# Kernel tuning notes

Measured on AMD Instinct MI355X. Metric: run time of the kernel, lower is better.

Reference implementation:

```python
import jax, jax.numpy as jnp
import numpy as np

B, N, IN_DIM, D, H = 8, 2048, 256, 512, 4
HD = D // H
GX, GY = 8, 8
IMG_W, IMG_H = 256.0, 256.0
CW, CH = IMG_W / GX, IMG_H / GY
NBH = 1
EPS = 1e-5


def setup_inputs() -> dict:
    key = jax.random.key(0)
    ks = jax.random.split(key, 12)
    s = 0.02
    rn = lambda k, sh: jax.random.normal(k, sh, jnp.float32) * s
    return {
        'features': jax.random.normal(ks[0], (B, N, IN_DIM), jnp.float32),
        'coords': jax.random.uniform(ks[1], (B, N, 2), jnp.float32) * IMG_W,
        'W_feat': rn(ks[2], (IN_DIM, D)), 'b_feat': jnp.zeros((D,), jnp.float32),
        'W_p1': rn(ks[3], (2, D // 2)), 'b_p1': jnp.zeros((D // 2,), jnp.float32),
        'W_p2': rn(ks[4], (D // 2, D)), 'b_p2': jnp.zeros((D,), jnp.float32),
        'Wq': rn(ks[5], (D, D)), 'bq': jnp.zeros((D,), jnp.float32),
        'Wk': rn(ks[6], (D, D)), 'bk': jnp.zeros((D,), jnp.float32),
        'Wv': rn(ks[7], (D, D)), 'bv': jnp.zeros((D,), jnp.float32),
        'Wo': rn(ks[8], (D, D)), 'bo': jnp.zeros((D,), jnp.float32),
        'gamma': jnp.ones((D,), jnp.float32), 'beta': jnp.zeros((D,), jnp.float32),
    }


def reference(features, coords, W_feat, b_feat, W_p1, b_p1, W_p2, b_p2,
              Wq, bq, Wk, bk, Wv, bv, Wo, bo, gamma, beta):
    feat = features @ W_feat + b_feat                          # [B,N,D]
    # --- grid bucketing (mean feature per occupied cell) ---
    gx = jnp.clip((coords[..., 0] / CW).astype(jnp.int32), 0, GX - 1)
    gy = jnp.clip((coords[..., 1] / CH).astype(jnp.int32), 0, GY - 1)
    cell = gx * GY + gy                                        # [B,N]
    G = GX * GY
    seg = (jnp.arange(B, dtype=jnp.int32)[:, None] * G + cell).reshape(-1)
    sums = jax.ops.segment_sum(feat.reshape(B * N, D), seg, num_segments=B * G)
    counts = jax.ops.segment_sum(jnp.ones((B * N,), jnp.float32), seg, num_segments=B * G)
    mean = (sums / jnp.maximum(counts, 1.0)[:, None]).reshape(B, G, D)
    counts = counts.reshape(B, G)
    # --- neighbor cells (static 3x3 window for neighborhood=1) ---
    offs = np.array([(dx, dy) for dx in range(-NBH, NBH + 1) for dy in range(-NBH, NBH + 1)], np.int32)
    K = offs.shape[0]
    pe = jnp.asarray(offs, jnp.float32)
    pe = jax.nn.relu(pe @ W_p1 + b_p1) @ W_p2 + b_p2           # [K,D] pos enc of offsets
    ngx = gx[..., None] + offs[:, 0]                           # [B,N,K]
    ngy = gy[..., None] + offs[:, 1]
    inb = (ngx >= 0) & (ngx < GX) & (ngy >= 0) & (ngy < GY)
    nidx = jnp.clip(ngx, 0, GX - 1) * GY + jnp.clip(ngy, 0, GY - 1)
    bidx = jnp.arange(B)[:, None, None]
    valid = inb & (counts[bidx, nidx] > 0)                     # [B,N,K]
    keys = mean[bidx, nidx] + pe                               # [B,N,K,D]
    # --- per-point attention over <=9 neighbor cells ---
    q = (feat @ Wq + bq).reshape(B, N, H, HD)
    k = (keys @ Wk + bk).reshape(B, N, K, H, HD)
    v = (keys @ Wv + bv).reshape(B, N, K, H, HD)
    scores = jnp.einsum('bnhd,bnkhd->bnhk', q, k) / np.float32(np.sqrt(HD))
    scores = jnp.where(valid[:, :, None, :], scores, jnp.float32(-1e9))
    attn = jax.nn.softmax(scores, axis=-1)
    agg = jnp.einsum('bnhk,bnkhd->bnhd', attn, v).reshape(B, N, D) @ Wo + bo
    enhanced = feat + agg                                      # residual (dropout in eval = identity)
    mu = enhanced.mean(-1, keepdims=True)
    var = enhanced.var(-1, keepdims=True)
    return (enhanced - mu) / jnp.sqrt(var + EPS) * gamma + beta
```

## Files before the change

kernel.cpp:

```cpp
#include <hip/hip_runtime.h>
#include <stdint.h>

typedef unsigned short u16;
typedef unsigned int u32;
typedef __bf16 bf16x8 __attribute__((ext_vector_type(8)));
typedef float f32x4 __attribute__((ext_vector_type(4)));

#define NBATCH 8
#define NPT    2048
#define NPTS   16384
#define INDIM  256
#define DD     512
#define GG     64

__device__ __forceinline__ u16 f2bf(float f){
  u32 u = __builtin_bit_cast(u32, f);
  u += 0x7fffu + ((u >> 16) & 1u);
  return (u16)(u >> 16);
}
__device__ __forceinline__ float bf2f(u16 h){
  u32 u = ((u32)h) << 16;
  return __builtin_bit_cast(float, u);
}
__device__ __forceinline__ void load8(const float* __restrict__ p, float* r){
  float4 a = *(const float4*)p;
  float4 b = *(const float4*)(p + 4);
  r[0]=a.x;r[1]=a.y;r[2]=a.z;r[3]=a.w;r[4]=b.x;r[5]=b.y;r[6]=b.z;r[7]=b.w;
}
__device__ __forceinline__ void load8bf(const u16* __restrict__ p, float* r){
  uint4 v = *(const uint4*)p;
  r[0]=bf2f((u16)v.x); r[1]=bf2f((u16)(v.x>>16));
  r[2]=bf2f((u16)v.y); r[3]=bf2f((u16)(v.y>>16));
  r[4]=bf2f((u16)v.z); r[5]=bf2f((u16)(v.z>>16));
  r[6]=bf2f((u16)v.w); r[7]=bf2f((u16)(v.w>>16));
}
__device__ __forceinline__ void store8(float* __restrict__ p, const float* r){
  float4 a; a.x=r[0];a.y=r[1];a.z=r[2];a.w=r[3];
  float4 b; b.x=r[4];b.y=r[5];b.z=r[6];b.w=r[7];
  *(float4*)p = a; *(float4*)(p+4) = b;
}
__device__ __forceinline__ uint4 pack8(const float* a){
  uint4 pk;
  pk.x = (u32)f2bf(a[0]) | ((u32)f2bf(a[1]) << 16);
  pk.y = (u32)f2bf(a[2]) | ((u32)f2bf(a[3]) << 16);
  pk.z = (u32)f2bf(a[4]) | ((u32)f2bf(a[5]) << 16);
  pk.w = (u32)f2bf(a[6]) | ((u32)f2bf(a[7]) << 16);
  return pk;
}
typedef __attribute__((address_space(1))) unsigned as1u;
typedef __attribute__((address_space(3))) unsigned as3u;
__device__ __forceinline__ void gload16(const void* g, void* l){
  __builtin_amdgcn_global_load_lds((as1u*)(uintptr_t)g, (as3u*)(uintptr_t)l, 16, 0, 0);
}

__device__ __forceinline__ void transpose64(const float* __restrict__ src, int scols,
                                            u16* __restrict__ dst, int dcols,
                                            int r0, int c0, char* smem, int t){
  float (*sh)[65] = (float(*)[65])smem;
  #pragma unroll
  for (int i = 0; i < 16; i++){
    int idx = i*256 + t;
    int r = idx >> 6, c = idx & 63;
    sh[r][c] = src[(size_t)(r0 + r)*scols + c0 + c];
  }
  __syncthreads();
  #pragma unroll
  for (int i = 0; i < 8; i++){
    int idx = i*512 + t*2;
    int oR = idx >> 6, oC = idx & 63;
    u32 pk = (u32)f2bf(sh[oC][oR]) | ((u32)f2bf(sh[oC+1][oR]) << 16);
    *(u32*)(dst + (size_t)(c0 + oR)*dcols + r0 + oC) = pk;
  }
}

#define P_R1 2048
#define P_R2 2112
#define P_R3 2368
#define P_R4 2400
#define P_R5 2409
#define P_R6 2411
#define P_R7 2415
#define P_NB 2423
__global__ __launch_bounds__(256) void prep_kernel(
    const float* __restrict__ features, const float* __restrict__ W_feat,
    const float* __restrict__ Wq, const float* __restrict__ Wk,
    const float* __restrict__ Wv, const float* __restrict__ Wo,
    const float* __restrict__ W_p1, const float* __restrict__ b_p1,
    const float* __restrict__ W_p2, const float* __restrict__ b_p2,
    const float* __restrict__ b_feat, const float* __restrict__ bq,
    const float* __restrict__ bk, const float* __restrict__ bv,
    const float* __restrict__ coords,
    u16* __restrict__ featA, u16* __restrict__ W_feat_bf,
    u16* __restrict__ WqkvT, u16* __restrict__ WoT, u16* __restrict__ WcatT,
    u16* __restrict__ peD, float* __restrict__ bfq, float* __restrict__ biaskv,
    int* __restrict__ order, int* __restrict__ counts, int* __restrict__ cellstart)
{
  __shared__ __align__(16) char smem[34048];
  int bid = blockIdx.x, t = threadIdx.x;
  if (bid < P_R1){
    int i = bid*256 + t;
    float r[8]; load8(features + (size_t)i*8, r);
    *(uint4*)(featA + (size_t)i*8) = pack8(r);
  } else if (bid < P_R2){
    int i = (bid - P_R1)*256 + t;
    float r[8]; load8(W_feat + (size_t)i*8, r);
    *(uint4*)(W_feat_bf + (size_t)i*8) = pack8(r);
  } else if (bid < P_R3){
    int rel = bid - P_R2;
    int mat = rel >> 6, tile = rel & 63;
    int r0 = (tile >> 3)*64, c0 = (tile & 7)*64;
    const float* src = mat==0 ? Wq : (mat==1 ? Wk : (mat==2 ? Wv : Wo));
    u16* dst = mat==0 ? WqkvT : (mat==1 ? WqkvT + (size_t)512*DD
                     : (mat==2 ? WqkvT + (size_t)1024*DD : WoT));
    transpose64(src, DD, dst, DD, r0, c0, smem, t);
  } else if (bid < P_R4){
    int rel = bid - P_R3;
    int r0 = (rel >> 3)*64, c0 = (rel & 7)*64;
    transpose64(W_feat, DD, WcatT, INDIM, r0, c0, smem, t);
  } else if (bid < P_R5){
    int kk = bid - P_R4;
    float dx = (float)(kk/3 - 1), dy = (float)(kk%3 - 1);
    float* h = (float*)smem;
    float hv = dx*W_p1[t] + dy*W_p1[256 + t] + b_p1[t];
    h[t] = hv > 0.f ? hv : 0.f;
    __syncthreads();
    float acc0 = b_p2[t], acc1 = b_p2[t + 256];
    for (int c = 0; c < 256; c++){
      float hc = h[c];
      acc0 += hc * W_p2[(size_t)c*DD + t];
      acc1 += hc * W_p2[(size_t)c*DD + t + 256];
    }
    peD[(size_t)kk*DD + t]       = f2bf(acc0);
    peD[(size_t)kk*DD + t + 256] = f2bf(acc1);
  } else if (bid < P_R6){
    int i = (bid - P_R5)*256 + t;
    float* bfs = (float*)smem;
    bfs[t] = b_feat[t]; bfs[t + 256] = b_feat[t + 256];
    __syncthreads();
    float acc = 0.f;
    for (int k = 0; k < DD; k++) acc += bfs[k] * Wq[(size_t)k*DD + i];
    bfq[i] = acc + bq[i];
  } else if (bid < P_R7){
    int n = (bid - P_R6)*256 + t;
    float* bfs = (float*)smem;
    bfs[t] = b_feat[t]; bfs[t + 256] = b_feat[t + 256];
    __syncthreads();
    const float* W = (n < 512) ? Wk : Wv;
    int c = n & 511;
    float acc = 0.f;
    for (int k = 0; k < DD; k++) acc += bfs[k] * W[(size_t)k*DD + c];
    biaskv[n] = acc + ((n < 512) ? bk[c] : bv[c]);
  } else {
    int b = bid - P_R7;
    u16 (*hist)[65] = (u16(*)[65])smem;
    int* tot  = (int*)(smem + 33280);
    int* base = (int*)(smem + 33536);
    #pragma unroll
    for (int i = 0; i < 65; i++) hist[t][i] = 0;
    int myc[8];
    float cxy[16];
    load8(coords + (size_t)(b*NPT + t*8)*2,     cxy);
    load8(coords + (size_t)(b*NPT + t*8)*2 + 8, cxy + 8);
    #pragma unroll
    for (int i = 0; i < 8; i++){
      int gx = (int)(cxy[2*i]   * (1.0f/32.0f)); gx = gx < 0 ? 0 : (gx > 7 ? 7 : gx);
      int gy = (int)(cxy[2*i+1] * (1.0f/32.0f)); gy = gy < 0 ? 0 : (gy > 7 ? 7 : gy);
      myc[i] = gx*8 + gy;
      hist[t][myc[i]]++;
    }
    __syncthreads();
    if (t < GG){
      int acc = 0;
      for (int tt = 0; tt < 256; tt++){ int v = hist[tt][t]; hist[tt][t] = (u16)acc; acc += v; }
      tot[t] = acc;
    }
    __syncthreads();
    if (t == 0){
      int acc = 0;
      for (int g = 0; g < GG; g++){ base[g] = acc; acc += tot[g]; }
    }
    __syncthreads();
    if (t < GG){
      counts[b*GG + t] = tot[t];
      cellstart[b*GG + t] = base[t];
    }
    #pragma unroll
    for (int i = 0; i < 8; i++){
      int g = myc[i];
      int local = 0;
      #pragma unroll
      for (int j = 0; j < 8; j++) local += (j < i && myc[j] == g) ? 1 : 0;
      order[b*NPT + base[g] + (int)hist[t][g] + local] = t*8 + i;
    }
  }
}

#define BM 128
#define BN 128
#define GEMM_PIPE(SMEMB, Aptr, Btptr, Kv, GXv, NWGv, UIDX)                         \
  u16* lA_ = (u16*)(SMEMB);                                                        \
  u16* lB_ = (u16*)((char*)(SMEMB) + 16384);                                       \
  int orig_ = (UIDX);                                                              \
  int swz_ = (orig_ & 7)*((NWGv) >> 3) + (orig_ >> 3);                             \
  int m0 = (swz_ / (GXv)) * BM, n0 = (swz_ % (GXv)) * BN;                          \
  int lane = tid & 63;                                                             \
  int wv = tid >> 6;                                                               \
  int wm = (wv >> 1) * 64, wn = (wv & 1) * 64;                                     \
  int lr = lane & 15;                                                              \
  int kg = (lane >> 4) << 3;                                                       \
  f32x4 acc[4][4] = {};                                                            \
  {                                                                                \
    int srow = lane >> 2;                                                          \
    int scol = (lane & 3) << 3;                                                    \
    const u16* gA0 = (Aptr)  + (size_t)(m0 + wv*32 + srow)*(Kv) + scol;            \
    const u16* gB0 = (Btptr) + (size_t)(n0 + wv*32 + srow)*(Kv) + scol;            \
    int lofs = (wv*32)*32;                                                         \
    int steps = (Kv) >> 5;                                                         \
    gload16(gA0,                   lA_ + lofs);                                    \
    gload16(gA0 + (size_t)16*(Kv), lA_ + lofs + 512);                              \
    gload16(gB0,                   lB_ + lofs);                                    \
    gload16(gB0 + (size_t)16*(Kv), lB_ + lofs + 512);                              \
    __syncthreads();                                                               \
    for (int s = 0; s < steps; s++){                                               \
      int cur = s & 1;                                                             \
      u16* lAc = lA_ + cur*4096;                                                   \
      u16* lBc = lB_ + cur*4096;                                                   \
      if (s + 1 < steps){                                                          \
        int kt = (s + 1) << 5;                                                     \
        u16* lAn = lA_ + (cur^1)*4096;                                             \
        u16* lBn = lB_ + (cur^1)*4096;                                             \
        gload16(gA0 + kt,                   lAn + lofs);                           \
        gload16(gA0 + kt + (size_t)16*(Kv), lAn + lofs + 512);                     \
        gload16(gB0 + kt,                   lBn + lofs);                           \
        gload16(gB0 + kt + (size_t)16*(Kv), lBn + lofs + 512);                     \
      }                                                                            \
      bf16x8 af[4], bfv[4];                                                        \
      _Pragma("unroll")                                                            \
      for (int i = 0; i < 4; i++) af[i]  = *(const bf16x8*)&lAc[(wm + i*16 + lr)*32 + kg]; \
      _Pragma("unroll")                                                            \
      for (int j = 0; j < 4; j++) bfv[j] = *(const bf16x8*)&lBc[(wn + j*16 + lr)*32 + kg]; \
      _Pragma("unroll")                                                            \
      for (int i = 0; i < 4; i++)                                                  \
        _Pragma("unroll")                                                          \
        for (int j = 0; j < 4; j++)                                                \
          acc[i][j] = __builtin_amdgcn_mfma_f32_16x16x32_bf16(af[i], bfv[j], acc[i][j], 0, 0, 0); \
      __syncthreads();                                                             \
    }                                                                              \
  }                                                                                \
  int lrow = (lane >> 4) << 2;

#define EPI_BF16(SMEMB, DST, LDN, BIAS)                                            \
  {                                                                                \
    u16* Cs = (u16*)(SMEMB);                                                       \
    _Pragma("unroll")                                                              \
    for (int j = 0; j < 4; j++){                                                   \
      int col = wn + j*16 + lr;                                                    \
      float bcol = (BIAS)[n0 + col];                                               \
      _Pragma("unroll")                                                            \
      for (int i = 0; i < 4; i++){                                                 \
        int r0 = wm + i*16 + lrow;                                                 \
        _Pragma("unroll")                                                          \
        for (int r = 0; r < 4; r++)                                                \
          Cs[(r0 + r)*136 + col] = f2bf(acc[i][j][r] + bcol);                      \
      }                                                                            \
    }                                                                              \
    __syncthreads();                                                               \
    _Pragma("unroll")                                                              \
    for (int k = 0; k < 8; k++){                                                   \
      int idx = k*256 + tid;                                                       \
      int row = idx >> 4, c8 = (idx & 15) << 3;                                    \
      *(uint4*)&(DST)[(size_t)(m0 + row)*(LDN) + n0 + c8] = *(uint4*)&Cs[row*136 + c8]; \
    }                                                                              \
  }

__global__ __launch_bounds__(256) void mid_kernel(
    const u16* __restrict__ WqkvT, const u16* __restrict__ W_feat_bf,
    const u16* __restrict__ peD, u16* __restrict__ Xout, float* __restrict__ meanKV,
    const u16* __restrict__ featA, const int* __restrict__ order,
    const int* __restrict__ counts, const int* __restrict__ cellstart,
    u16* __restrict__ meanF, const u16* __restrict__ WcatT,
    const float* __restrict__ b_feat, u16* __restrict__ feat_bf)
{
  __shared__ __align__(16) char SMEM[34816];
  int tid = threadIdx.x;
  if (blockIdx.x < 24){
    GEMM_PIPE(SMEM, WqkvT, W_feat_bf, 512, 2, 24, (int)blockIdx.x)
    #pragma unroll
    for (int j = 0; j < 4; j++){
      int col = n0 + wn + j*16 + lr;
      #pragma unroll
      for (int i = 0; i < 4; i++){
        int row0 = m0 + wm + i*16 + lrow;
        #pragma unroll
        for (int r = 0; r < 4; r++)
          Xout[(size_t)(row0 + r)*INDIM + col] = f2bf(acc[i][j][r]);
      }
    }
  } else if (blockIdx.x < 60){
    float* pesh = (float*)SMEM;
    int bid2 = blockIdx.x - 24;
    int kk = bid2 >> 2, seg = bid2 & 3;
    int n = seg*256 + tid;
    pesh[tid]       = bf2f(peD[(size_t)kk*DD + tid]);
    pesh[tid + 256] = bf2f(peD[(size_t)kk*DD + tid + 256]);
    __syncthreads();
    const u16* wrow = WqkvT + (size_t)(512 + n)*DD;
    float acc = 0.f;
    for (int d8 = 0; d8 < 64; d8++){
      float w8[8]; load8bf(wrow + d8*8, w8);
      #pragma unroll
      for (int j = 0; j < 8; j++) acc += pesh[d8*8 + j]*w8[j];
    }
    meanKV[(size_t)(512 + kk)*1024 + n] = acc;
  } else if (blockIdx.x < 572){
    float (*part)[2] = (float(*)[2])SMEM;
    int bg = blockIdx.x - 60;
    int b = bg >> 6;
    int p = tid & 127, half = tid >> 7;
    int cnt = counts[bg], start = cellstart[bg];
    const int* ord = order + b*NPT + start;
    float a0 = 0.f, a1 = 0.f;
    for (int n = half; n < cnt; n += 2){
      u32 v = *(const u32*)(featA + (((size_t)(b*NPT + ord[n])) << 8) + p*2);
      a0 += bf2f((u16)v); a1 += bf2f((u16)(v >> 16));
    }
    if (half){ part[p][0] = a0; part[p][1] = a1; }
    __syncthreads();
    if (!half){
      a0 += part[p][0]; a1 += part[p][1];
      float inv = 1.f / (float)(cnt > 0 ? cnt : 1);
      *(u32*)(meanF + (size_t)bg*INDIM + p*2) =
          (u32)f2bf(a0*inv) | ((u32)f2bf(a1*inv) << 16);
    }
  } else {
    GEMM_PIPE(SMEM, featA, WcatT, 256, 4, 512, (int)blockIdx.x - 572)
    EPI_BF16(SMEM, feat_bf, DD, b_feat)
  }
}

__global__ __launch_bounds__(256) void qmean_kernel(
    const u16* __restrict__ featA, const u16* __restrict__ WfqT,
    const u16* __restrict__ meanF, const u16* __restrict__ WfkvT,
    const float* __restrict__ bfq, const float* __restrict__ biaskv,
    u16* __restrict__ q_bf, float* __restrict__ meanKV)
{
  __shared__ __align__(16) char SMEM[34816];
  int tid = threadIdx.x;
  if (blockIdx.x < 512){
    GEMM_PIPE(SMEM, featA, WfqT, 256, 4, 512, (int)blockIdx.x)
    EPI_BF16(SMEM, q_bf, DD, bfq)
  } else {
    GEMM_PIPE(SMEM, meanF, WfkvT, 256, 8, 32, (int)blockIdx.x - 512)
    #pragma unroll
    for (int j = 0; j < 4; j++){
      int col = n0 + wn + j*16 + lr;
      float bcol = biaskv[col];
      #pragma unroll
      for (int i = 0; i < 4; i++){
        int row0 = m0 + wm + i*16 + lrow;
        #pragma unroll
        for (int r = 0; r < 4; r++)
          meanKV[(size_t)(row0 + r)*1024 + col] = acc[i][j][r] + bcol;
      }
    }
  }
}

__global__ __launch_bounds__(1024) void attn_cells(
    const u16* __restrict__ q, const float* __restrict__ meanKV,
    const int* __restrict__ order, const int* __restrict__ counts,
    const int* __restrict__ cellstart, u16* __restrict__ agg)
{
  int bg = blockIdx.x;
  int b = bg >> 6, c = bg & 63;
  int gx = c >> 3, gy = c & 7;
  __shared__ __align__(16) u16 Kf[9][DD];
  __shared__ __align__(16) u16 Vf[9][DD];
  __shared__ int vrow[9];
  int t = threadIdx.x;
  if (t < 9){
    int dx = t/3 - 1, dy = t%3 - 1;
    int nx = gx + dx, ny = gy + dy;
    int inb = ((unsigned)nx < 8u) && ((unsigned)ny < 8u);
    int row = b*GG + (((nx&7) << 3) | (ny&7));
    vrow[t] = (inb && counts[row] > 0) ? row : -1;
  }
  __syncthreads();
  int d = 2*(t & 255);
  for (int kk = (t >> 8); kk < 9; kk += 4){
    int row = vrow[kk];
    if (row >= 0){
      float2 mk = *(const float2*)&meanKV[(size_t)row*1024 + d];
      float2 pk = *(const float2*)&meanKV[(size_t)(512+kk)*1024 + d];
      float2 mv = *(const float2*)&meanKV[(size_t)row*1024 + 512 + d];
      float2 pv = *(const float2*)&meanKV[(size_t)(512+kk)*1024 + 512 + d];
      *(u32*)&Kf[kk][d] = (u32)f2bf(mk.x+pk.x) | ((u32)f2bf(mk.y+pk.y) << 16);
      *(u32*)&Vf[kk][d] = (u32)f2bf(mv.x+pv.x) | ((u32)f2bf(mv.y+pv.y) << 16);
    }
  }
  __syncthreads();
  int cnt = counts[bg];
  int wv = t >> 6, lane = t & 63;
  const int* ord = order + b*NPT + cellstart[bg];
  for (int i = wv; i < cnt; i += 16){
    size_t p = (size_t)b*NPT + ord[i];
    float qv[8];
    load8bf(q + p*DD + lane*8, qv);
    float s[9];
    #pragma unroll
    for (int kk = 0; kk < 9; kk++){
      float partial = 0.f;
      if (vrow[kk] >= 0){
        float kv[8]; load8bf(&Kf[kk][lane*8], kv);
        #pragma unroll
        for (int j = 0; j < 8; j++) partial += qv[j]*kv[j];
      }
      partial += __shfl_xor(partial, 1);
      partial += __shfl_xor(partial, 2);
      partial += __shfl_xor(partial, 4);
      partial += __shfl_xor(partial, 8);
      s[kk] = (vrow[kk] >= 0) ? partial * 0.08838834764831843f : -1e30f;
    }
    float mx = s[0];
    #pragma unroll
    for (int kk = 1; kk < 9; kk++) mx = fmaxf(mx, s[kk]);
    float w[9], sum = 0.f;
    #pragma unroll
    for (int kk = 0; kk < 9; kk++){
      w[kk] = (vrow[kk] >= 0) ? __expf(s[kk] - mx) : 0.f;
      sum += w[kk];
    }
    float inv = 1.f / sum;
    float a[8] = {0,0,0,0,0,0,0,0};
    #pragma unroll
    for (int kk = 0; kk < 9; kk++){
      if (vrow[kk] >= 0){
        float wk = w[kk] * inv;
        float vv[8]; load8bf(&Vf[kk][lane*8], vv);
        #pragma unroll
        for (int j = 0; j < 8; j++) a[j] += wk*vv[j];
      }
    }
    *(uint4*)&agg[p*DD + lane*8] = pack8(a);
  }
}

__global__ __launch_bounds__(256) void lin_kernel(
    const u16* __restrict__ agg_bf, const u16* __restrict__ WoT,
    const float* __restrict__ bo, u16* __restrict__ lin_bf)
{
  __shared__ __align__(16) char SMEM[34816];
  int tid = threadIdx.x;
  GEMM_PIPE(SMEM, agg_bf, WoT, 512, 4, 512, (int)blockIdx.x)
  EPI_BF16(SMEM, lin_bf, DD, bo)
}

__global__ __launch_bounds__(256) void ln_kernel(
    const u16* __restrict__ feat, const u16* __restrict__ lin,
    const float* __restrict__ gamma, const float* __restrict__ beta,
    float* __restrict__ out)
{
  int wv = threadIdx.x >> 6, lane = threadIdx.x & 63;
  size_t r = (size_t)blockIdx.x * 4 + wv;
  int d0 = lane * 8;
  float fv[8], lv[8];
  load8bf(feat + r*DD + d0, fv);
  load8bf(lin  + r*DD + d0, lv);
  float e[8], s1 = 0.f, s2 = 0.f;
  #pragma unroll
  for (int j = 0; j < 8; j++){ e[j] = fv[j] + lv[j]; s1 += e[j]; s2 += e[j]*e[j]; }
  #pragma unroll
  for (int m = 1; m < 64; m <<= 1){ s1 += __shfl_xor(s1, m); s2 += __shfl_xor(s2, m); }
  float mu  = s1 * (1.f/512.f);
  float var = s2 * (1.f/512.f) - mu*mu;
  float istd = rsqrtf(var + 1e-5f);
  float gv[8], bev[8];
  load8(gamma + d0, gv); load8(beta + d0, bev);
  float o[8];
  #pragma unroll
  for (int j = 0; j < 8; j++) o[j] = (e[j] - mu)*istd*gv[j] + bev[j];
  store8(out + r*DD + d0, o);
}

extern "C" void kernel_launch(void* const* d_in, const int* in_sizes, int n_in,
                              void* d_out, int out_size, void* d_ws, size_t ws_size,
                              hipStream_t stream) {
  (void)in_sizes; (void)n_in; (void)out_size; (void)ws_size;
  const float* features = (const float*)d_in[0];
  const float* coords   = (const float*)d_in[1];
  const float* W_feat   = (const float*)d_in[2];
  const float* b_feat   = (const float*)d_in[3];
  const float* W_p1     = (const float*)d_in[4];
  const float* b_p1     = (const float*)d_in[5];
  const float* W_p2     = (const float*)d_in[6];
  const float* b_p2     = (const float*)d_in[7];
  const float* Wq = (const float*)d_in[8];  const float* bq = (const float*)d_in[9];
  const float* Wk = (const float*)d_in[10]; const float* bk = (const float*)d_in[11];
  const float* Wv = (const float*)d_in[12]; const float* bv = (const float*)d_in[13];
  const float* Wo = (const float*)d_in[14]; const float* bo = (const float*)d_in[15];
  const float* gamma = (const float*)d_in[16]; const float* beta = (const float*)d_in[17];
  float* out = (float*)d_out;

  char* ws = (char*)d_ws;
  size_t off = 0;
  auto alloc = [&](size_t bytes) -> void* {
    void* p = ws + off;
    off = (off + bytes + 255) & ~(size_t)255;
    return p;
  };
  u16*   featA     = (u16*)  alloc((size_t)NPTS*INDIM*2);
  u16*   feat_bf   = (u16*)  alloc((size_t)NPTS*DD*2);
  u16*   q_bf      = (u16*)  alloc((size_t)NPTS*DD*2);
  u16*   agg_bf    = (u16*)  alloc((size_t)NPTS*DD*2);
  u16*   lin_bf    = (u16*)  alloc((size_t)NPTS*DD*2);
  u16*   W_feat_bf = (u16*)  alloc((size_t)INDIM*DD*2);
  u16*   WqkvT     = (u16*)  alloc((size_t)1536*DD*2);
  u16*   WoT       = (u16*)  alloc((size_t)DD*DD*2);
  u16*   WcatT     = (u16*)  alloc((size_t)512*INDIM*2);
  u16*   Xout      = (u16*)  alloc((size_t)1536*INDIM*2);
  u16*   peD       = (u16*)  alloc((size_t)9*DD*2);
  u16*   meanF     = (u16*)  alloc((size_t)512*INDIM*2);
  float* meanKV    = (float*)alloc((size_t)640*1024*4);
  float* bfq       = (float*)alloc((size_t)DD*4);
  float* biaskv    = (float*)alloc((size_t)1024*4);
  int*   order     = (int*)  alloc((size_t)NPTS*4);
  int*   counts    = (int*)  alloc((size_t)NBATCH*GG*4);
  int*   cellstart = (int*)  alloc((size_t)NBATCH*GG*4);
  u16*   WfqT      = Xout;
  u16*   WfkvT     = Xout + (size_t)512*INDIM;

  prep_kernel<<<P_NB, 256, 0, stream>>>(
      features, W_feat, Wq, Wk, Wv, Wo, W_p1, b_p1, W_p2, b_p2,
      b_feat, bq, bk, bv, coords,
      featA, W_feat_bf, WqkvT, WoT, WcatT, peD, bfq, biaskv,
      order, counts, cellstart);
  mid_kernel<<<1084, 256, 0, stream>>>(
      WqkvT, W_feat_bf, peD, Xout, meanKV, featA, order, counts, cellstart,
      meanF, WcatT, b_feat, feat_bf);
  qmean_kernel<<<544, 256, 0, stream>>>(
      featA, WfqT, meanF, WfkvT, bfq, biaskv, q_bf, meanKV);
  attn_cells<<<NBATCH*GG, 1024, 0, stream>>>(q_bf, meanKV, order, counts, cellstart, agg_bf);
  lin_kernel<<<512, 256, 0, stream>>>(agg_bf, WoT, bo, lin_bf);
  ln_kernel<<<NPTS/4, 256, 0, stream>>>(feat_bf, lin_bf, gamma, beta, out);
}
```

Before: 102.8 us.

## Fuse output projection GEMM with residual LayerNorm in one kernel

Replaces the separate Wo projection GEMM and LayerNorm kernels with one kernel. Each 512-thread block computes a full 64x512 output row tile with MFMA, stages it in LDS as bf16, then applies residual add and LayerNorm directly. This removes the lin_bf global round trip and one launch. The cost is fewer blocks (256 instead of 512), a large 72KB LDS footprint that limits occupancy, and the whole B matrix being streamed per block.

```diff
diff --git a/kernel.cpp b/kernel.cpp
--- a/kernel.cpp
+++ b/kernel.cpp
@@ -28,6 +28,13 @@
   r[0]=a.x;r[1]=a.y;r[2]=a.z;r[3]=a.w;r[4]=b.x;r[5]=b.y;r[6]=b.z;r[7]=b.w;
 }
 __device__ __forceinline__ void load8bf(const u16* __restrict__ p, float* r){
+  uint4 v = *(const uint4*)p;
+  r[0]=bf2f((u16)v.x); r[1]=bf2f((u16)(v.x>>16));
+  r[2]=bf2f((u16)v.y); r[3]=bf2f((u16)(v.y>>16));
+  r[4]=bf2f((u16)v.z); r[5]=bf2f((u16)(v.z>>16));
+  r[6]=bf2f((u16)v.w); r[7]=bf2f((u16)(v.w>>16));
+}
+__device__ __forceinline__ void load8bf_lds(const u16* p, float* r){
   uint4 v = *(const uint4*)p;
   r[0]=bf2f((u16)v.x); r[1]=bf2f((u16)(v.x>>16));
   r[2]=bf2f((u16)v.y); r[3]=bf2f((u16)(v.y>>16));
@@ -445,41 +452,99 @@
   }
 }
 
-__global__ __launch_bounds__(256) void lin_kernel(
+__global__ __launch_bounds__(512) void linln_kernel(
     const u16* __restrict__ agg_bf, const u16* __restrict__ WoT,
-    const float* __restrict__ bo, u16* __restrict__ lin_bf)
-{
-  __shared__ __align__(16) char SMEM[34816];
-  int tid = threadIdx.x;
-  GEMM_PIPE(SMEM, agg_bf, WoT, 512, 4, 512, (int)blockIdx.x)
-  EPI_BF16(SMEM, lin_bf, DD, bo)
-}
-
-__global__ __launch_bounds__(256) void ln_kernel(
-    const u16* __restrict__ feat, const u16* __restrict__ lin,
+    const float* __restrict__ bo, const u16* __restrict__ feat_bf,
     const float* __restrict__ gamma, const float* __restrict__ beta,
     float* __restrict__ out)
 {
-  int wv = threadIdx.x >> 6, lane = threadIdx.x & 63;
-  size_t r = (size_t)blockIdx.x * 4 + wv;
-  int d0 = lane * 8;
-  float fv[8], lv[8];
-  load8bf(feat + r*DD + d0, fv);
-  load8bf(lin  + r*DD + d0, lv);
-  float e[8], s1 = 0.f, s2 = 0.f;
+  __shared__ __align__(16) char SMEM[73728];
+  u16* lA = (u16*)SMEM;
+  u16* lB = (u16*)(SMEM + 8192);
+  int tid = threadIdx.x;
+  int lane = tid & 63;
+  int wvv = tid >> 6;
+  int m0 = blockIdx.x * 64;
+  int wm2 = (wvv >> 2) * 32;
+  int wn2 = (wvv & 3) * 128;
+  int lr = lane & 15;
+  int kg = (lane >> 4) << 3;
+  int srow = lane >> 2;
+  int scol = (lane & 3) << 3;
+  f32x4 acc[2][8] = {};
+  {
+    const u16* gB0 = WoT + (size_t)(wvv*64 + srow)*DD + scol;
+    int lBoff = (wvv*64)*32;
+    const u16* gA0 = agg_bf + (size_t)(m0 + (wvv&3)*16 + srow)*DD + scol;
+    int lAoff = ((wvv&3)*16)*32;
+    bool doA = (wvv < 4);
+    #pragma unroll
+    for (int c = 0; c < 4; c++)
+      gload16(gB0 + (size_t)(c*16)*DD, lB + lBoff + c*16*32);
+    if (doA) gload16(gA0, lA + lAoff);
+    __syncthreads();
+    for (int s = 0; s < 16; s++){
+      int cur = s & 1;
+      u16* lAc = lA + cur*2048;
+      u16* lBc = lB + cur*16384;
+      if (s + 1 < 16){
+        int kt = (s + 1) << 5;
+        u16* lAn = lA + (cur^1)*2048;
+        u16* lBn = lB + (cur^1)*16384;
+        #pragma unroll
+        for (int c = 0; c < 4; c++)
+          gload16(gB0 + kt + (size_t)(c*16)*DD, lBn + lBoff + c*16*32);
+        if (doA) gload16(gA0 + kt, lAn + lAoff);
+      }
+      bf16x8 af[2], bfv[8];
+      #pragma unroll
+      for (int i = 0; i < 2; i++) af[i]  = *(const bf16x8*)&lAc[(wm2 + i*16 + lr)*32 + kg];
+      #pragma unroll
+      for (int j = 0; j < 8; j++) bfv[j] = *(const bf16x8*)&lBc[(wn2 + j*16 + lr)*32 + kg];
+      #pragma unroll
+      for (int i = 0; i < 2; i++)
+        #pragma unroll
+        for (int j = 0; j < 8; j++)
+          acc[i][j] = __builtin_amdgcn_mfma_f32_16x16x32_bf16(af[i], bfv[j], acc[i][j], 0, 0, 0);
+      __syncthreads();
+    }
+  }
+  int lrow = (lane >> 4) << 2;
+  u16* Cs = (u16*)SMEM;
   #pragma unroll
-  for (int j = 0; j < 8; j++){ e[j] = fv[j] + lv[j]; s1 += e[j]; s2 += e[j]*e[j]; }
-  #pragma unroll
-  for (int m = 1; m < 64; m <<= 1){ s1 += __shfl_xor(s1, m); s2 += __shfl_xor(s2, m); }
-  float mu  = s1 * (1.f/512.f);
-  float var = s2 * (1.f/512.f) - mu*mu;
-  float istd = rsqrtf(var + 1e-5f);
+  for (int j = 0; j < 8; j++){
+    int col = wn2 + j*16 + lr;
+    float bcol = bo[col];
+    #pragma unroll
+    for (int i = 0; i < 2; i++){
+      int r0 = wm2 + i*16 + lrow;
+      #pragma unroll
+      for (int r = 0; r < 4; r++)
+        Cs[(r0 + r)*520 + col] = f2bf(acc[i][j][r] + bcol);
+    }
+  }
+  __syncthreads();
   float gv[8], bev[8];
-  load8(gamma + d0, gv); load8(beta + d0, bev);
-  float o[8];
-  #pragma unroll
-  for (int j = 0; j < 8; j++) o[j] = (e[j] - mu)*istd*gv[j] + bev[j];
-  store8(out + r*DD + d0, o);
+  load8(gamma + lane*8, gv);
+  load8(beta + lane*8, bev);
+  for (int rr = 0; rr < 8; rr++){
+    int row = wvv*8 + rr;
+    float lv[8], fv[8];
+    load8bf_lds(&Cs[row*520 + lane*8], lv);
+    load8bf(feat_bf + (size_t)(m0 + row)*DD + lane*8, fv);
+    float e[8], s1 = 0.f, s2 = 0.f;
+    #pragma unroll
+    for (int j = 0; j < 8; j++){ e[j] = fv[j] + lv[j]; s1 += e[j]; s2 += e[j]*e[j]; }
+    #pragma unroll
+    for (int m = 1; m < 64; m <<= 1){ s1 += __shfl_xor(s1, m); s2 += __shfl_xor(s2, m); }
+    float mu  = s1 * (1.f/512.f);
+    float var = s2 * (1.f/512.f) - mu*mu;
+    float istd = rsqrtf(var + 1e-5f);
+    float o[8];
+    #pragma unroll
+    for (int j = 0; j < 8; j++) o[j] = (e[j] - mu)*istd*gv[j] + bev[j];
+    store8(out + (size_t)(m0 + row)*DD + lane*8, o);
+  }
 }
 
 extern "C" void kernel_launch(void* const* d_in, const int* in_sizes, int n_in,
@@ -512,7 +577,6 @@
   u16*   feat_bf   = (u16*)  alloc((size_t)NPTS*DD*2);
   u16*   q_bf      = (u16*)  alloc((size_t)NPTS*DD*2);
   u16*   agg_bf    = (u16*)  alloc((size_t)NPTS*DD*2);
-  u16*   lin_bf    = (u16*)  alloc((size_t)NPTS*DD*2);
   u16*   W_feat_bf = (u16*)  alloc((size_t)INDIM*DD*2);
   u16*   WqkvT     = (u16*)  alloc((size_t)1536*DD*2);
   u16*   WoT       = (u16*)  alloc((size_t)DD*DD*2);
@@ -540,6 +604,5 @@
   qmean_kernel<<<544, 256, 0, stream>>>(
       featA, WfqT, meanF, WfkvT, bfq, biaskv, q_bf, meanKV);
   attn_cells<<<NBATCH*GG, 1024, 0, stream>>>(q_bf, meanKV, order, counts, cellstart, agg_bf);
-  lin_kernel<<<512, 256, 0, stream>>>(agg_bf, WoT, bo, lin_bf);
-  ln_kernel<<<NPTS/4, 256, 0, stream>>>(feat_bf, lin_bf, gamma, beta, out);
-}
+  linln_kernel<<<NPTS/64, 512, 0, stream>>>(agg_bf, WoT, bo, feat_bf, gamma, beta, out);
+}
```

Measured after the change: 101.8 us, median of 3. Within noise of the previous version (-1.0%).
